# Kernel tuning notes

Hardware: AMD Instinct MI355X
Metric: run time of the kernel (lower is better)

## Reference

```python
import jax, jax.numpy as jnp
import numpy as np

B, N, D, H, DEG = 2, 20000, 256, 8, 8
E = N * DEG
EPS = 1e-3  # keras LayerNormalization default epsilon


def layer_norm(x, gamma, beta):
    mu = jnp.mean(x, axis=-1, keepdims=True)
    var = jnp.mean(jnp.square(x - mu), axis=-1, keepdims=True)
    return (x - mu) * jax.lax.rsqrt(var + EPS) * gamma + beta


def setup_inputs() -> dict:
    key = jax.random.key(0)
    ks = jax.random.split(key, 8)
    x = jax.random.normal(ks[0], (B, N, D), dtype=jnp.float32)
    # edge list sorted by source node; every node has DEG out-edges so
    # segment_sum covers all N segments (matches tf.math.segment_sum semantics)
    src = jnp.repeat(jnp.arange(N, dtype=jnp.int64), DEG)
    dst = jax.random.randint(ks[1], (E,), 0, N, dtype=jnp.int64)
    edges = jnp.stack([src, dst], axis=1)  # [E, 2]
    scale = 0.05
    wq = jax.random.normal(ks[2], (D, D), dtype=jnp.float32) * scale
    wk = jax.random.normal(ks[3], (D, D), dtype=jnp.float32) * scale
    wv = jax.random.normal(ks[4], (D, D), dtype=jnp.float32) * scale
    wo = jax.random.normal(ks[5], (D, D), dtype=jnp.float32) * scale
    zeros = jnp.zeros((D,), dtype=jnp.float32)
    ones = jnp.ones((D,), dtype=jnp.float32)
    return {
        "x": x, "edges": edges,
        "wq": wq, "bq": zeros, "wk": wk, "bk": zeros,
        "wv": wv, "bv": zeros, "wo": wo, "bo": zeros,
        "gamma1": ones, "beta1": zeros, "gamma2": ones, "beta2": zeros,
    }


def reference(x, edges, wq, bq, wk, bk, wv, bv, wo, bo, gamma1, beta1, gamma2, beta2):
    b, n, d = x.shape
    h, dh = H, D // H
    xn = layer_norm(x, gamma1, beta1)                      # [B,N,D]
    # QKV projections, split heads, move node axis to front: [N,B,H,dh]
    def proj(w, bias):
        y = (xn @ w + bias).reshape(b, n, h, dh)
        return jnp.transpose(y, (1, 0, 2, 3))
    q, k, v = proj(wq, bq), proj(wk, bk), proj(wv, bv)
    src, dst = edges[:, 0], edges[:, 1]
    q_part = q[src]                                         # [E,B,H,dh]
    k_part = k[dst]
    v_part = v[dst]
    logits = jnp.sum(q_part * k_part, axis=-1, keepdims=True) / jnp.sqrt(
        jnp.asarray(dh, dtype=x.dtype))                     # [E,B,H,1]
    w = jnp.exp(logits)                                     # unnormalized softmax (as in source)
    num = jax.ops.segment_sum(v_part * w, src, num_segments=n)  # [N,B,H,dh]
    den = jax.ops.segment_sum(w, src, num_segments=n)           # [N,B,H,1]
    attn = num / den
    attn = jnp.transpose(attn, (1, 0, 2, 3)).reshape(b, n, d)   # [B,N,D]
    concat = xn + attn                                      # residual uses normed input (source reassigns `inputs`)
    out = layer_norm(concat, gamma2, beta2)
    out = jax.nn.relu(out @ wo + bo)
    return out + concat
```

## Files before the change

### kernel.cpp

```cpp
#include <hip/hip_runtime.h>


typedef __bf16 bf16x8 __attribute__((ext_vector_type(8)));
typedef float  f32x4  __attribute__((ext_vector_type(4)));

__device__ __forceinline__ float bf2f(unsigned short u) {
    union { unsigned int i; float f; } v; v.i = ((unsigned int)u) << 16; return v.f;
}
__device__ __forceinline__ unsigned short f2bf(float f) {
    union { float f; unsigned int i; } v; v.f = f;
    unsigned int x = v.i;
    unsigned int r = (x + 0x7FFFu + ((x >> 16) & 1u)) >> 16;
    return (unsigned short)r;
}

#define NNODE 20000
#define ROWS  40000
#define DMODEL 256

__global__ __launch_bounds__(256) void prep_ln1_kernel(
    const float* __restrict__ wq, const float* __restrict__ wk,
    const float* __restrict__ wv, const float* __restrict__ wo,
    const float* __restrict__ bq, const float* __restrict__ bk,
    const float* __restrict__ bv, const float* __restrict__ bo,
    const float* __restrict__ x,
    const float* __restrict__ g1, const float* __restrict__ b1,
    unsigned short* __restrict__ Wqkvt,
    unsigned short* __restrict__ Wot,
    float* __restrict__ biasq,
    float* __restrict__ biaso,
    unsigned short* __restrict__ xn)
{
    if (blockIdx.x < 1024) {
        int idx = blockIdx.x * 256 + threadIdx.x;
        if (idx < 768 * 256) {
            int n = idx >> 8, k = idx & 255;
            int sel = n >> 8, nl = n & 255;
            const float* w = (sel == 0) ? wq : (sel == 1) ? wk : wv;
            Wqkvt[idx] = f2bf(w[k * 256 + nl]);
        } else {
            int idx2 = idx - 768 * 256;
            int n = idx2 >> 8, k = idx2 & 255;
            Wot[idx2] = f2bf(wo[k * 256 + n]);
        }
        if (idx < 768) {
            const float* bb = (idx < 256) ? bq : (idx < 512) ? bk : bv;
            biasq[idx] = bb[idx & 255];
        }
        if (idx >= 768 && idx < 1024) biaso[idx - 768] = bo[idx - 768];
        return;
    }
    int wave = threadIdx.x >> 6, lane = threadIdx.x & 63;
    int sub = lane >> 5, hl = lane & 31;
    int m = (blockIdx.x - 1024) * 8 + wave * 2 + sub;
    const float* xp = x + (size_t)m * DMODEL + hl * 8;
    float4 x0 = *(const float4*)xp;
    float4 x1 = *(const float4*)(xp + 4);
    float f[8] = {x0.x, x0.y, x0.z, x0.w, x1.x, x1.y, x1.z, x1.w};
    float s = 0.f, ss = 0.f;
    #pragma unroll
    for (int t = 0; t < 8; ++t) { s += f[t]; ss += f[t]*f[t]; }
    #pragma unroll
    for (int mk = 1; mk < 32; mk <<= 1) { s += __shfl_xor(s, mk); ss += __shfl_xor(ss, mk); }
    float mu  = s * (1.f/256.f);
    float var = ss * (1.f/256.f) - mu*mu;
    float rs  = rsqrtf(var + 1e-3f);
    float4 g0 = *(const float4*)(g1 + hl * 8);
    float4 g1v = *(const float4*)(g1 + hl * 8 + 4);
    float4 b0 = *(const float4*)(b1 + hl * 8);
    float4 b1v = *(const float4*)(b1 + hl * 8 + 4);
    float gg[8] = {g0.x, g0.y, g0.z, g0.w, g1v.x, g1v.y, g1v.z, g1v.w};
    float bb[8] = {b0.x, b0.y, b0.z, b0.w, b1v.x, b1v.y, b1v.z, b1v.w};
    unsigned short o[8];
    #pragma unroll
    for (int t = 0; t < 8; ++t) o[t] = f2bf((f[t] - mu) * rs * gg[t] + bb[t]);
    *(int4*)(xn + (size_t)m * DMODEL + hl * 8) = *(const int4*)o;
}

#define LDS_W 72
#define MFMA_BF16(d, a, b) d = __builtin_amdgcn_mfma_f32_16x16x32_bf16(a, b, d, 0, 0, 0)

template<bool EPI>
__global__ __launch_bounds__(256, 2) void gemm_kernel(
    const unsigned short* __restrict__ A,
    const unsigned short* __restrict__ Bt,
    const float* __restrict__ bias,
    void* __restrict__ C,
    const unsigned short* __restrict__ resid,
    int M, int Ncols)
{
    __shared__ unsigned short As[128 * LDS_W];
    __shared__ unsigned short Bs[128 * LDS_W];
    int tid  = threadIdx.x;
    int wave = tid >> 6, lane = tid & 63;
    int quad = lane >> 4, l16 = lane & 15;

    int nt_total = Ncols >> 7;
    int nwg = gridDim.x;
    int xcd = blockIdx.x & 7, loc = blockIdx.x >> 3;
    int qq = nwg >> 3, rr = nwg & 7;
    int wid = (xcd < rr) ? (xcd * (qq + 1) + loc)
                         : (rr * (qq + 1) + (xcd - rr) * qq + loc);
    int mt = wid / nt_total;
    int nt = wid - mt * nt_total;
    int m0 = mt * 128, n0 = nt * 128;
    int wm = (wave >> 1) * 64, wn = (wave & 1) * 64;

    int srow = tid >> 1;
    int sseg = (tid & 1) * 32;
    int arow = m0 + srow; if (arow >= M) arow = M - 1;
    const unsigned short* ArowP = A  + (size_t)arow * 256 + sseg;
    const unsigned short* BrowP = Bt + (size_t)(n0 + srow) * 256 + sseg;
    unsigned short* AsP = &As[srow * LDS_W + sseg];
    unsigned short* BsP = &Bs[srow * LDS_W + sseg];

    f32x4 acc00 = {}, acc01 = {}, acc02 = {}, acc03 = {};
    f32x4 acc10 = {}, acc11 = {}, acc12 = {}, acc13 = {};
    f32x4 acc20 = {}, acc21 = {}, acc22 = {}, acc23 = {};
    f32x4 acc30 = {}, acc31 = {}, acc32 = {}, acc33 = {};

    int4 va0 = *(const int4*)(ArowP);
    int4 va1 = *(const int4*)(ArowP + 8);
    int4 va2 = *(const int4*)(ArowP + 16);
    int4 va3 = *(const int4*)(ArowP + 24);
    int4 vb0 = *(const int4*)(BrowP);
    int4 vb1 = *(const int4*)(BrowP + 8);
    int4 vb2 = *(const int4*)(BrowP + 16);
    int4 vb3 = *(const int4*)(BrowP + 24);

    for (int kt = 0; kt < 4; ++kt) {
        __syncthreads();
        *(int4*)(AsP)      = va0;
        *(int4*)(AsP + 8)  = va1;
        *(int4*)(AsP + 16) = va2;
        *(int4*)(AsP + 24) = va3;
        *(int4*)(BsP)      = vb0;
        *(int4*)(BsP + 8)  = vb1;
        *(int4*)(BsP + 16) = vb2;
        *(int4*)(BsP + 24) = vb3;
        __syncthreads();
        if (kt < 3) {
            const unsigned short* ap = ArowP + (kt + 1) * 64;
            const unsigned short* bp = BrowP + (kt + 1) * 64;
            va0 = *(const int4*)(ap);
            va1 = *(const int4*)(ap + 8);
            va2 = *(const int4*)(ap + 16);
            va3 = *(const int4*)(ap + 24);
            vb0 = *(const int4*)(bp);
            vb1 = *(const int4*)(bp + 8);
            vb2 = *(const int4*)(bp + 16);
            vb3 = *(const int4*)(bp + 24);
        }
        #pragma unroll
        for (int ks = 0; ks < 64; ks += 32) {
            bf16x8 a0 = *(const bf16x8*)&As[(wm +  0 + l16) * LDS_W + ks + quad * 8];
            bf16x8 a1 = *(const bf16x8*)&As[(wm + 16 + l16) * LDS_W + ks + quad * 8];
            bf16x8 a2 = *(const bf16x8*)&As[(wm + 32 + l16) * LDS_W + ks + quad * 8];
            bf16x8 a3 = *(const bf16x8*)&As[(wm + 48 + l16) * LDS_W + ks + quad * 8];
            bf16x8 b0 = *(const bf16x8*)&Bs[(wn +  0 + l16) * LDS_W + ks + quad * 8];
            bf16x8 b1 = *(const bf16x8*)&Bs[(wn + 16 + l16) * LDS_W + ks + quad * 8];
            bf16x8 b2 = *(const bf16x8*)&Bs[(wn + 32 + l16) * LDS_W + ks + quad * 8];
            bf16x8 b3 = *(const bf16x8*)&Bs[(wn + 48 + l16) * LDS_W + ks + quad * 8];
            MFMA_BF16(acc00, a0, b0); MFMA_BF16(acc01, a0, b1);
            MFMA_BF16(acc02, a0, b2); MFMA_BF16(acc03, a0, b3);
            MFMA_BF16(acc10, a1, b0); MFMA_BF16(acc11, a1, b1);
            MFMA_BF16(acc12, a1, b2); MFMA_BF16(acc13, a1, b3);
            MFMA_BF16(acc20, a2, b0); MFMA_BF16(acc21, a2, b1);
            MFMA_BF16(acc22, a2, b2); MFMA_BF16(acc23, a2, b3);
            MFMA_BF16(acc30, a3, b0); MFMA_BF16(acc31, a3, b1);
            MFMA_BF16(acc32, a3, b2); MFMA_BF16(acc33, a3, b3);
        }
    }

#define EPI_STORE(accv, R, CC) do {                                          \
        int col = n0 + wn + (CC) * 16 + l16;                                 \
        float bb = bias[col];                                                \
        int rowb = m0 + wm + (R) * 16 + quad * 4;                            \
        _Pragma("unroll")                                                    \
        for (int rr = 0; rr < 4; ++rr) {                                     \
            int row = rowb + rr;                                             \
            if (row < M) {                                                   \
                float v = (accv)[rr] + bb;                                   \
                if (EPI) {                                                   \
                    v = fmaxf(v, 0.f);                                       \
                    v += bf2f(resid[(size_t)row * 256 + col]);               \
                    ((float*)C)[(size_t)row * Ncols + col] = v;              \
                } else {                                                     \
                    ((unsigned short*)C)[(size_t)row * Ncols + col] = f2bf(v);\
                }                                                            \
            }                                                                \
        }                                                                    \
    } while (0)

    EPI_STORE(acc00, 0, 0); EPI_STORE(acc01, 0, 1); EPI_STORE(acc02, 0, 2); EPI_STORE(acc03, 0, 3);
    EPI_STORE(acc10, 1, 0); EPI_STORE(acc11, 1, 1); EPI_STORE(acc12, 1, 2); EPI_STORE(acc13, 1, 3);
    EPI_STORE(acc20, 2, 0); EPI_STORE(acc21, 2, 1); EPI_STORE(acc22, 2, 2); EPI_STORE(acc23, 2, 3);
    EPI_STORE(acc30, 3, 0); EPI_STORE(acc31, 3, 1); EPI_STORE(acc32, 3, 2); EPI_STORE(acc33, 3, 3);
#undef EPI_STORE
}

__global__ __launch_bounds__(256) void attn_kernel(
    const unsigned short* __restrict__ qkv,
    const int* __restrict__ edges,
    const unsigned short* __restrict__ xn,
    const float* __restrict__ g2, const float* __restrict__ b2,
    unsigned short* __restrict__ concat,
    unsigned short* __restrict__ h2)
{
    int wave = threadIdx.x >> 6, lane = threadIdx.x & 63;
    int i = blockIdx.x * 4 + wave;
    int b = lane >> 5, hl = lane & 31;
    size_t m = (size_t)b * NNODE + i;

    int4 qi = *(const int4*)(qkv + m * 768 + hl * 8);
    int4 xi = *(const int4*)(xn + m * DMODEL + hl * 8);
    const unsigned short* qs = (const unsigned short*)&qi;
    float qf[8];
    #pragma unroll
    for (int t = 0; t < 8; ++t) qf[t] = bf2f(qs[t]);

    int jv = 0;
    if (lane < 8) jv = edges[2 * (i * 8 + lane) + 1];

#define KVLOAD(E)                                                                  \
    int j##E = __shfl(jv, E);                                                      \
    const unsigned short* kp##E = qkv + ((size_t)b * NNODE + j##E) * 768 + 256 + hl * 8; \
    int4 KI##E = *(const int4*)(kp##E);                                            \
    int4 VI##E = *(const int4*)(kp##E + 256);
    KVLOAD(0) KVLOAD(1) KVLOAD(2) KVLOAD(3)
    KVLOAD(4) KVLOAD(5) KVLOAD(6) KVLOAD(7)
#undef KVLOAD

    float acc[8] = {};
    float den = 0.f;
    const float scale = 0.17677669529663687f;
#define EDGE(E) do {                                                         \
        const unsigned short* ks = (const unsigned short*)&KI##E;            \
        const unsigned short* vs = (const unsigned short*)&VI##E;            \
        float dot = 0.f;                                                     \
        _Pragma("unroll")                                                    \
        for (int t = 0; t < 8; ++t) dot += qf[t] * bf2f(ks[t]);              \
        dot += __shfl_xor(dot, 1);                                           \
        dot += __shfl_xor(dot, 2);               \
        float w = __expf(dot * scale);                                       \
        _Pragma("unroll")                                                    \
        for (int t = 0; t < 8; ++t) acc[t] += w * bf2f(vs[t]);               \
        den += w;                                                            \
    } while (0)
    EDGE(0); EDGE(1); EDGE(2); EDGE(3);
    EDGE(4); EDGE(5); EDGE(6); EDGE(7);
#undef EDGE
    float inv = 1.f / den;

    const unsigned short* xs = (const unsigned short*)&xi;
    float c[8], s = 0.f, ss = 0.f;
    #pragma unroll
    for (int t = 0; t < 8; ++t) { c[t] = bf2f(xs[t]) + acc[t] * inv; s += c[t]; ss += c[t]*c[t]; }
    #pragma unroll
    for (int mk = 1; mk < 32; mk <<= 1) { s += __shfl_xor(s, mk); ss += __shfl_xor(ss, mk); }
    float mu  = s * (1.f/256.f);
    float var = ss * (1.f/256.f) - mu*mu;
    float rs  = rsqrtf(var + 1e-3f);

    float4 ga = *(const float4*)(g2 + hl * 8);
    float4 gb = *(const float4*)(g2 + hl * 8 + 4);
    float4 ba = *(const float4*)(b2 + hl * 8);
    float4 bb = *(const float4*)(b2 + hl * 8 + 4);
    float gg[8] = {ga.x, ga.y, ga.z, ga.w, gb.x, gb.y, gb.z, gb.w};
    float bv[8] = {ba.x, ba.y, ba.z, ba.w, bb.x, bb.y, bb.z, bb.w};
    unsigned short oc[8], oh[8];
    #pragma unroll
    for (int t = 0; t < 8; ++t) {
        oc[t] = f2bf(c[t]);
        oh[t] = f2bf((c[t] - mu) * rs * gg[t] + bv[t]);
    }
    *(int4*)(concat + m * DMODEL + hl * 8) = *(const int4*)oc;
    *(int4*)(h2     + m * DMODEL + hl * 8) = *(const int4*)oh;
}

extern "C" void kernel_launch(void* const* d_in, const int* in_sizes, int n_in,
                              void* d_out, int out_size, void* d_ws, size_t ws_size,
                              hipStream_t stream)
{
    const float* x   = (const float*)d_in[0];
    const int* edges = (const int*)d_in[1];
    const float* wq = (const float*)d_in[2];
    const float* bq = (const float*)d_in[3];
    const float* wk = (const float*)d_in[4];
    const float* bk = (const float*)d_in[5];
    const float* wv = (const float*)d_in[6];
    const float* bv = (const float*)d_in[7];
    const float* wo = (const float*)d_in[8];
    const float* bo = (const float*)d_in[9];
    const float* g1 = (const float*)d_in[10];
    const float* b1 = (const float*)d_in[11];
    const float* g2 = (const float*)d_in[12];
    const float* b2 = (const float*)d_in[13];

    char* ws = (char*)d_ws;
    unsigned short* Wqkvt = (unsigned short*)(ws);
    unsigned short* Wot   = (unsigned short*)(ws + 393216);
    float* biasq          = (float*)(ws + 393216 + 131072);
    float* biaso          = (float*)(ws + 393216 + 131072 + 3072);
    size_t off = 393216 + 131072 + 4096;
    unsigned short* xn     = (unsigned short*)(ws + off); off += (size_t)ROWS * DMODEL * 2;
    unsigned short* qkv    = (unsigned short*)(ws + off); off += (size_t)ROWS * 768 * 2;
    unsigned short* concat = (unsigned short*)(ws + off); off += (size_t)ROWS * DMODEL * 2;
    unsigned short* h2     = (unsigned short*)(ws + off); off += (size_t)ROWS * DMODEL * 2;

    prep_ln1_kernel<<<1024 + ROWS / 8, 256, 0, stream>>>(
        wq, wk, wv, wo, bq, bk, bv, bo, x, g1, b1, Wqkvt, Wot, biasq, biaso, xn);
    gemm_kernel<false><<<dim3(313 * 6), 256, 0, stream>>>(xn, Wqkvt, biasq, qkv, nullptr, ROWS, 768);
    attn_kernel<<<NNODE / 4, 256, 0, stream>>>(qkv, edges, xn, g2, b2, concat, h2);
    gemm_kernel<true><<<dim3(313 * 2), 256, 0, stream>>>(h2, Wot, biaso, d_out, concat, ROWS, 256);
}
```

Baseline: 228.9 us.

## Interleave batch rows, double-buffer swizzled GEMM LDS tiles

Reorders intermediate rows so both batch entries of a node sit next to each other. The attention kernel's gathered K/V reads for the two batches then fall in adjacent 1.5KB rows, which should improve cache and DRAM locality. The final store maps rows back to the original layout. The GEMM switches from padded LDS rows to an XOR-swizzled layout with double buffering, which drops one barrier per k-step and overlaps the LDS stores with the MFMAs, at the cost of doubling LDS use.

```diff
diff --git a/kernel.cpp b/kernel.cpp
--- a/kernel.cpp
+++ b/kernel.cpp
@@ -53,7 +53,8 @@
     int wave = threadIdx.x >> 6, lane = threadIdx.x & 63;
     int sub = lane >> 5, hl = lane & 31;
     int m = (blockIdx.x - 1024) * 8 + wave * 2 + sub;
-    const float* xp = x + (size_t)m * DMODEL + hl * 8;
+    int crow = (m & 1) * NNODE + (m >> 1);
+    const float* xp = x + (size_t)crow * DMODEL + hl * 8;
     float4 x0 = *(const float4*)xp;
     float4 x1 = *(const float4*)(xp + 4);
     float f[8] = {x0.x, x0.y, x0.z, x0.w, x1.x, x1.y, x1.z, x1.w};
@@ -77,8 +78,8 @@
     *(int4*)(xn + (size_t)m * DMODEL + hl * 8) = *(const int4*)o;
 }
 
-#define LDS_W 72
 #define MFMA_BF16(d, a, b) d = __builtin_amdgcn_mfma_f32_16x16x32_bf16(a, b, d, 0, 0, 0)
+#define SWZI(r, c) (((r) << 6) + ((c) ^ (((r) & 7) << 3)))
 
 template<bool EPI>
 __global__ __launch_bounds__(256, 2) void gemm_kernel(
@@ -89,8 +90,8 @@
     const unsigned short* __restrict__ resid,
     int M, int Ncols)
 {
-    __shared__ unsigned short As[128 * LDS_W];
-    __shared__ unsigned short Bs[128 * LDS_W];
+    __shared__ __align__(16) unsigned short As[2 * 128 * 64];
+    __shared__ __align__(16) unsigned short Bs[2 * 128 * 64];
     int tid  = threadIdx.x;
     int wave = tid >> 6, lane = tid & 63;
     int quad = lane >> 4, l16 = lane & 15;
@@ -111,8 +112,10 @@
     int arow = m0 + srow; if (arow >= M) arow = M - 1;
     const unsigned short* ArowP = A  + (size_t)arow * 256 + sseg;
     const unsigned short* BrowP = Bt + (size_t)(n0 + srow) * 256 + sseg;
-    unsigned short* AsP = &As[srow * LDS_W + sseg];
-    unsigned short* BsP = &Bs[srow * LDS_W + sseg];
+    int wi0 = SWZI(srow, sseg + 0);
+    int wi1 = SWZI(srow, sseg + 8);
+    int wi2 = SWZI(srow, sseg + 16);
+    int wi3 = SWZI(srow, sseg + 24);
 
     f32x4 acc00 = {}, acc01 = {}, acc02 = {}, acc03 = {};
     f32x4 acc10 = {}, acc11 = {}, acc12 = {}, acc13 = {};
@@ -127,40 +130,38 @@
     int4 vb1 = *(const int4*)(BrowP + 8);
     int4 vb2 = *(const int4*)(BrowP + 16);
     int4 vb3 = *(const int4*)(BrowP + 24);
-
+    *(int4*)&As[wi0] = va0;
+    *(int4*)&As[wi1] = va1;
+    *(int4*)&As[wi2] = va2;
+    *(int4*)&As[wi3] = va3;
+    *(int4*)&Bs[wi0] = vb0;
+    *(int4*)&Bs[wi1] = vb1;
+    *(int4*)&Bs[wi2] = vb2;
+    *(int4*)&Bs[wi3] = vb3;
+    va0 = *(const int4*)(ArowP + 64);
+    va1 = *(const int4*)(ArowP + 72);
+    va2 = *(const int4*)(ArowP + 80);
+    va3 = *(const int4*)(ArowP + 88);
+    vb0 = *(const int4*)(BrowP + 64);
+    vb1 = *(const int4*)(BrowP + 72);
+    vb2 = *(const int4*)(BrowP + 80);
+    vb3 = *(const int4*)(BrowP + 88);
+    __syncthreads();
+
+    #pragma unroll
     for (int kt = 0; kt < 4; ++kt) {
-        __syncthreads();
-        *(int4*)(AsP)      = va0;
-        *(int4*)(AsP + 8)  = va1;
-        *(int4*)(AsP + 16) = va2;
-        *(int4*)(AsP + 24) = va3;
-        *(int4*)(BsP)      = vb0;
-        *(int4*)(BsP + 8)  = vb1;
-        *(int4*)(BsP + 16) = vb2;
-        *(int4*)(BsP + 24) = vb3;
-        __syncthreads();
-        if (kt < 3) {
-            const unsigned short* ap = ArowP + (kt + 1) * 64;
-            const unsigned short* bp = BrowP + (kt + 1) * 64;
-            va0 = *(const int4*)(ap);
-            va1 = *(const int4*)(ap + 8);
-            va2 = *(const int4*)(ap + 16);
-            va3 = *(const int4*)(ap + 24);
-            vb0 = *(const int4*)(bp);
-            vb1 = *(const int4*)(bp + 8);
-            vb2 = *(const int4*)(bp + 16);
-            vb3 = *(const int4*)(bp + 24);
-        }
+        int cb = (kt & 1) << 13;
         #pragma unroll
         for (int ks = 0; ks < 64; ks += 32) {
-            bf16x8 a0 = *(const bf16x8*)&As[(wm +  0 + l16) * LDS_W + ks + quad * 8];
-            bf16x8 a1 = *(const bf16x8*)&As[(wm + 16 + l16) * LDS_W + ks + quad * 8];
-            bf16x8 a2 = *(const bf16x8*)&As[(wm + 32 + l16) * LDS_W + ks + quad * 8];
-            bf16x8 a3 = *(const bf16x8*)&As[(wm + 48 + l16) * LDS_W + ks + quad * 8];
-            bf16x8 b0 = *(const bf16x8*)&Bs[(wn +  0 + l16) * LDS_W + ks + quad * 8];
-            bf16x8 b1 = *(const bf16x8*)&Bs[(wn + 16 + l16) * LDS_W + ks + quad * 8];
-            bf16x8 b2 = *(const bf16x8*)&Bs[(wn + 32 + l16) * LDS_W + ks + quad * 8];
-            bf16x8 b3 = *(const bf16x8*)&Bs[(wn + 48 + l16) * LDS_W + ks + quad * 8];
+            int ca = ks + quad * 8;
+            bf16x8 a0 = *(const bf16x8*)&As[cb + SWZI(wm +  0 + l16, ca)];
+            bf16x8 a1 = *(const bf16x8*)&As[cb + SWZI(wm + 16 + l16, ca)];
+            bf16x8 a2 = *(const bf16x8*)&As[cb + SWZI(wm + 32 + l16, ca)];
+            bf16x8 a3 = *(const bf16x8*)&As[cb + SWZI(wm + 48 + l16, ca)];
+            bf16x8 b0 = *(const bf16x8*)&Bs[cb + SWZI(wn +  0 + l16, ca)];
+            bf16x8 b1 = *(const bf16x8*)&Bs[cb + SWZI(wn + 16 + l16, ca)];
+            bf16x8 b2 = *(const bf16x8*)&Bs[cb + SWZI(wn + 32 + l16, ca)];
+            bf16x8 b3 = *(const bf16x8*)&Bs[cb + SWZI(wn + 48 + l16, ca)];
             MFMA_BF16(acc00, a0, b0); MFMA_BF16(acc01, a0, b1);
             MFMA_BF16(acc02, a0, b2); MFMA_BF16(acc03, a0, b3);
             MFMA_BF16(acc10, a1, b0); MFMA_BF16(acc11, a1, b1);
@@ -169,6 +170,30 @@
             MFMA_BF16(acc22, a2, b2); MFMA_BF16(acc23, a2, b3);
             MFMA_BF16(acc30, a3, b0); MFMA_BF16(acc31, a3, b1);
             MFMA_BF16(acc32, a3, b2); MFMA_BF16(acc33, a3, b3);
+        }
+        if (kt < 3) {
+            int nb = ((kt + 1) & 1) << 13;
+            *(int4*)&As[nb + wi0] = va0;
+            *(int4*)&As[nb + wi1] = va1;
+            *(int4*)&As[nb + wi2] = va2;
+            *(int4*)&As[nb + wi3] = va3;
+            *(int4*)&Bs[nb + wi0] = vb0;
+            *(int4*)&Bs[nb + wi1] = vb1;
+            *(int4*)&Bs[nb + wi2] = vb2;
+            *(int4*)&Bs[nb + wi3] = vb3;
+            if (kt < 2) {
+                const unsigned short* ap = ArowP + (kt + 2) * 64;
+                const unsigned short* bp = BrowP + (kt + 2) * 64;
+                va0 = *(const int4*)(ap);
+                va1 = *(const int4*)(ap + 8);
+                va2 = *(const int4*)(ap + 16);
+                va3 = *(const int4*)(ap + 24);
+                vb0 = *(const int4*)(bp);
+                vb1 = *(const int4*)(bp + 8);
+                vb2 = *(const int4*)(bp + 16);
+                vb3 = *(const int4*)(bp + 24);
+            }
+            __syncthreads();
         }
     }
 
@@ -184,7 +209,8 @@
                 if (EPI) {                                                   \
                     v = fmaxf(v, 0.f);                                       \
                     v += bf2f(resid[(size_t)row * 256 + col]);               \
-                    ((float*)C)[(size_t)row * Ncols + col] = v;              \
+                    int crow = (row & 1) * NNODE + (row >> 1);               \
+                    ((float*)C)[(size_t)crow * Ncols + col] = v;             \
                 } else {                                                     \
                     ((unsigned short*)C)[(size_t)row * Ncols + col] = f2bf(v);\
                 }                                                            \
@@ -210,7 +236,7 @@
     int wave = threadIdx.x >> 6, lane = threadIdx.x & 63;
     int i = blockIdx.x * 4 + wave;
     int b = lane >> 5, hl = lane & 31;
-    size_t m = (size_t)b * NNODE + i;
+    size_t m = (size_t)i * 2 + b;
 
     int4 qi = *(const int4*)(qkv + m * 768 + hl * 8);
     int4 xi = *(const int4*)(xn + m * DMODEL + hl * 8);
@@ -224,7 +250,7 @@
 
 #define KVLOAD(E)                                                                  \
     int j##E = __shfl(jv, E);                                                      \
-    const unsigned short* kp##E = qkv + ((size_t)b * NNODE + j##E) * 768 + 256 + hl * 8; \
+    const unsigned short* kp##E = qkv + ((size_t)j##E * 2 + b) * 768 + 256 + hl * 8; \
     int4 KI##E = *(const int4*)(kp##E);                                            \
     int4 VI##E = *(const int4*)(kp##E + 256);
     KVLOAD(0) KVLOAD(1) KVLOAD(2) KVLOAD(3)
```

After: 244.7 us. +6.9%, slower.
